# Kernel tuning notes

Measured on AMD Instinct MI355X. Metric: run time of the kernel, lower is better.

The kernel has to match this reference:

```python
import jax, jax.numpy as jnp
import numpy as np

OFF_SLOPE = 0.001

def setup_inputs() -> dict:
    key = jax.random.key(0)
    B, S, I, H = 128, 1024, 128, 256
    ks = jax.random.split(key, 8)
    stdv = 1.0 / np.sqrt(H)
    x = jax.random.normal(ks[0], (B, S, I), dtype=jnp.float32)
    # monotone positive timestamps per sequence
    ts = jnp.sort(jax.random.uniform(ks[1], (B, S), jnp.float32, 0.0, 1000.0), axis=1)
    W = jax.random.uniform(ks[2], (I, 4 * H), jnp.float32, -stdv, stdv)
    U = jax.random.uniform(ks[3], (H, 4 * H), jnp.float32, -stdv, stdv)
    bias = jax.random.uniform(ks[4], (4 * H,), jnp.float32, -stdv, stdv)
    # Periods = exp(2*rand + 1), Shifts ~ U(0,100), On_End = 0.05 (per init_weights)
    Periods = jnp.exp(2.0 * jax.random.uniform(ks[5], (H, 1), jnp.float32) + 1.0)
    Shifts = jax.random.uniform(ks[6], (H, 1), jnp.float32, 0.0, 100.0)
    On_End = jnp.full((H, 1), 0.05, dtype=jnp.float32)
    return {"x": x, "ts": ts, "W": W, "U": U, "bias": bias,
            "Periods": Periods, "Shifts": Shifts, "On_End": On_End}

def reference(x, ts, W, U, bias, Periods, Shifts, On_End):
    B, S, I = x.shape
    H = U.shape[0]
    shift = Shifts.reshape(1, -1)                 # [1,H]
    period = jnp.abs(Periods.reshape(1, -1))      # [1,H]
    on_mid = jnp.abs(On_End.reshape(1, -1)) * 0.5 * period
    on_end = jnp.abs(On_End.reshape(1, -1)) * period

    def step(carry, inp):
        h, c = carry
        x_t, t_t = inp                            # [B,I], [B]
        gates = x_t @ W + h @ U + bias            # [B,4H]
        i_g, f_g, g_g, o_g = jnp.split(gates, 4, axis=-1)
        i_t = jax.nn.sigmoid(i_g)
        f_t = jax.nn.sigmoid(f_g)
        g_t = jnp.tanh(g_g)
        o_t = jax.nn.sigmoid(o_g)
        c_new = f_t * c + i_t * g_t
        h_new = o_t * jnp.tanh(c_new)
        # phased time gate
        in_cycle = jnp.fmod(t_t[:, None] + shift, period)   # [B,H]
        is_up = in_cycle <= on_mid
        is_down = (in_cycle > on_mid) & (in_cycle <= on_end)
        mask = jnp.where(is_up, in_cycle / on_mid,
                         jnp.where(is_down, (on_end - in_cycle) / on_mid,
                                   OFF_SLOPE * (in_cycle / period)))
        c2 = mask * c_new + (1.0 - mask) * c
        h2 = mask * h_new + (1.0 - mask) * h
        return (h2, c2), h2

    h0 = jnp.zeros((B, H), x.dtype)
    c0 = jnp.zeros((B, H), x.dtype)
    (h_T, c_T), hs = jax.lax.scan(
        step, (h0, c0), (jnp.swapaxes(x, 0, 1), jnp.swapaxes(ts, 0, 1)))
    hidden_seq = jnp.swapaxes(hs, 0, 1)           # [B,S,H]
    return hidden_seq, h_T, c_T
```

## Files before the change

kernel.cpp:

```cpp
#include <hip/hip_runtime.h>
#include <cstdint>
#include <cstddef>

#define B_ 128
#define S_ 1024
#define I_ 128
#define H_ 256
#define G4 1024
#define OFF_SLOPE 0.001f

typedef float f32x4 __attribute__((ext_vector_type(4)));
typedef short s16x8 __attribute__((ext_vector_type(8)));

__device__ __forceinline__ unsigned short f2bf_rne(float f) {
    unsigned int u = __builtin_bit_cast(unsigned int, f);
    u += 0x7FFFu + ((u >> 16) & 1u);
    return (unsigned short)(u >> 16);
}
__device__ __forceinline__ float bf2f(unsigned short h) {
    unsigned int u = ((unsigned int)h) << 16;
    return __builtin_bit_cast(float, u);
}
__device__ __forceinline__ float fsigmoid(float x) {
    return 1.0f / (1.0f + __expf(-x));
}
__device__ __forceinline__ float ftanh(float x) {
    return 2.0f / (1.0f + __expf(-2.0f * x)) - 1.0f;
}

template <bool SCANLAYOUT>
__global__ __launch_bounds__(256) void gemm_xw(const float* __restrict__ X,
                                               const float* __restrict__ W,
                                               const float* __restrict__ bias,
                                               float* __restrict__ Gx) {
    __shared__ float A_s[16 * 128];
    const int tid = threadIdx.x;
    const size_t row0 = (size_t)blockIdx.x * 16;

    for (int i = tid; i < 16 * 128; i += 256)
        A_s[i] = X[row0 * I_ + i];
    __syncthreads();

    const float4 bias4 = ((const float4*)bias)[tid];
    float4 acc[16];
#pragma unroll
    for (int r = 0; r < 16; ++r) acc[r] = bias4;

    const float4* W4 = (const float4*)W;
    for (int k = 0; k < I_; ++k) {
        float4 w = W4[k * 256 + tid];
#pragma unroll
        for (int r = 0; r < 16; ++r) {
            float a = A_s[r * 128 + k];
            acc[r].x = fmaf(a, w.x, acc[r].x);
            acc[r].y = fmaf(a, w.y, acc[r].y);
            acc[r].z = fmaf(a, w.z, acc[r].z);
            acc[r].w = fmaf(a, w.w, acc[r].w);
        }
    }
    if (SCANLAYOUT) {
        const int b = (int)(row0 >> 10);
        const int t0 = (int)(row0 & 1023);
        const int g = b >> 4, bb = b & 15;
        const int n0 = 4 * tid;
        const int q = n0 >> 8, u = n0 & 255, cb = u >> 5, j = u & 31;
        const int lc = q * 32 + j;
#pragma unroll
        for (int r = 0; r < 16; ++r) {
            size_t idx = ((((size_t)(g * 8 + cb) * 1024 + (t0 + r)) * 16 + bb) * 128 + lc);
            *(float4*)&Gx[idx] = acc[r];
        }
    } else {
        float4* O4 = (float4*)Gx;
#pragma unroll
        for (int r = 0; r < 16; ++r)
            O4[(row0 + r) * 256 + tid] = acc[r];
    }
}

__global__ __launch_bounds__(256, 1) void plstm_mfma(
    const float* __restrict__ ts, const float* __restrict__ U,
    const float* __restrict__ Periods, const float* __restrict__ Shifts,
    const float* __restrict__ OnEnd, const float* __restrict__ Gx,
    float* __restrict__ out, unsigned long long* __restrict__ hbuf,
    int* __restrict__ ctr) {
    const int blk = blockIdx.x;
    const int g = blk & 7;
    const int cb = blk >> 3;
    const int tid = threadIdx.x;
    const int w = tid >> 6;
    const int l = tid & 63;
    const int lr = l & 15;
    const int lg = l >> 4;

    __shared__ unsigned short h_hi[16 * 264];
    __shared__ unsigned short h_lo[16 * 264];
    __shared__ float gates[4 * 16 * 33];

    s16x8 Uhi[2][8], Ulo[2][8];
#pragma unroll
    for (int tt = 0; tt < 2; ++tt) {
        const int n = w * 256 + cb * 32 + tt * 16 + lr;
#pragma unroll
        for (int kk = 0; kk < 8; ++kk) {
            s16x8 hi8, lo8;
#pragma unroll
            for (int i = 0; i < 8; ++i) {
                int k = kk * 32 + lg * 8 + i;
                float uv = U[(size_t)k * G4 + n];
                unsigned short h = f2bf_rne(uv);
                float r = uv - bf2f(h);
                hi8[i] = (short)h;
                lo8[i] = (short)f2bf_rne(r);
            }
            Uhi[tt][kk] = hi8;
            Ulo[tt][kk] = lo8;
        }
    }

    const int eb = tid >> 4;
    const int ej = 2 * (tid & 15);
    const int u0 = cb * 32 + ej;
    const float per0 = fabsf(Periods[u0]), per1 = fabsf(Periods[u0 + 1]);
    const float sh0 = Shifts[u0], sh1 = Shifts[u0 + 1];
    const float oe0 = fabsf(OnEnd[u0]) * per0, oe1 = fabsf(OnEnd[u0 + 1]) * per1;
    const float om0 = 0.5f * oe0, om1 = 0.5f * oe1;
    const float iom0 = 1.0f / om0, iom1 = 1.0f / om1;
    const float ip0 = 1.0f / per0, ip1 = 1.0f / per1;

    float c0 = 0.f, c1 = 0.f, h0 = 0.f, h1 = 0.f;
    const float* tsrow = ts + (size_t)(g * 16 + eb) * S_;
    const float* gxbase = Gx + (size_t)(g * 8 + cb) * 1024 * 2048 + eb * 128;
    float* outrow = out + (size_t)(g * 16 + eb) * S_ * H_ + u0;

    unsigned long long* const hb0 = hbuf + (size_t)g * 2048;
    unsigned long long* const hb1 = hbuf + (size_t)(8 + g) * 2048;

    for (int i = tid; i < 16 * 264; i += 256) { h_hi[i] = 0; h_lo[i] = 0; }
    __syncthreads();

    const int abase = lr * 264 + lg * 8;
    const int pubidx = eb * 128 + cb * 16 + (tid & 15);
    const int b2 = tid >> 4, seg = tid & 15;
    const int rbase = b2 * 128 + seg * 8;

    float2 cq0 = *(const float2*)&gxbase[0 * 32 + ej];
    float2 cq1 = *(const float2*)&gxbase[1 * 32 + ej];
    float2 cq2 = *(const float2*)&gxbase[2 * 32 + ej];
    float2 cq3 = *(const float2*)&gxbase[3 * 32 + ej];
    float tsc = tsrow[0];

    for (int t = 0; t < S_; ++t) {
        f32x4 a0 = {0.f, 0.f, 0.f, 0.f}, a1 = {0.f, 0.f, 0.f, 0.f};
#pragma unroll
        for (int kk = 0; kk < 8; ++kk) {
            s16x8 ah = *(const s16x8*)&h_hi[abase + kk * 32];
            s16x8 al = *(const s16x8*)&h_lo[abase + kk * 32];
            a0 = __builtin_amdgcn_mfma_f32_16x16x32_bf16(ah, Uhi[0][kk], a0, 0, 0, 0);
            a0 = __builtin_amdgcn_mfma_f32_16x16x32_bf16(ah, Ulo[0][kk], a0, 0, 0, 0);
            a0 = __builtin_amdgcn_mfma_f32_16x16x32_bf16(al, Uhi[0][kk], a0, 0, 0, 0);
            a1 = __builtin_amdgcn_mfma_f32_16x16x32_bf16(ah, Uhi[1][kk], a1, 0, 0, 0);
            a1 = __builtin_amdgcn_mfma_f32_16x16x32_bf16(ah, Ulo[1][kk], a1, 0, 0, 0);
            a1 = __builtin_amdgcn_mfma_f32_16x16x32_bf16(al, Uhi[1][kk], a1, 0, 0, 0);
        }
#pragma unroll
        for (int r = 0; r < 4; ++r) {
            gates[(w * 16 + lg * 4 + r) * 33 + lr] = a0[r];
            gates[(w * 16 + lg * 4 + r) * 33 + 16 + lr] = a1[r];
        }
        __syncthreads();

        float i0 = gates[(0 * 16 + eb) * 33 + ej] + cq0.x;
        float f0 = gates[(1 * 16 + eb) * 33 + ej] + cq1.x;
        float g0 = gates[(2 * 16 + eb) * 33 + ej] + cq2.x;
        float o0 = gates[(3 * 16 + eb) * 33 + ej] + cq3.x;
        float i1 = gates[(0 * 16 + eb) * 33 + ej + 1] + cq0.y;
        float f1 = gates[(1 * 16 + eb) * 33 + ej + 1] + cq1.y;
        float g1 = gates[(2 * 16 + eb) * 33 + ej + 1] + cq2.y;
        float o1 = gates[(3 * 16 + eb) * 33 + ej + 1] + cq3.y;

        float it0 = fsigmoid(i0), ft0 = fsigmoid(f0);
        float gt0 = ftanh(g0), ot0 = fsigmoid(o0);
        float it1 = fsigmoid(i1), ft1 = fsigmoid(f1);
        float gt1 = ftanh(g1), ot1 = fsigmoid(o1);

        float cn0 = fmaf(ft0, c0, it0 * gt0);
        float hn0 = ot0 * ftanh(cn0);
        float cn1 = fmaf(ft1, c1, it1 * gt1);
        float hn1 = ot1 * ftanh(cn1);

        float ic0 = fmodf(tsc + sh0, per0);
        float m0 = (ic0 <= om0) ? ic0 * iom0
                 : (ic0 <= oe0) ? (oe0 - ic0) * iom0
                                : OFF_SLOPE * (ic0 * ip0);
        float ic1 = fmodf(tsc + sh1, per1);
        float m1 = (ic1 <= om1) ? ic1 * iom1
                 : (ic1 <= oe1) ? (oe1 - ic1) * iom1
                                : OFF_SLOPE * (ic1 * ip1);

        c0 = m0 * cn0 + (1.f - m0) * c0;
        c1 = m1 * cn1 + (1.f - m1) * c1;
        h0 = m0 * hn0 + (1.f - m0) * h0;
        h1 = m1 * hn1 + (1.f - m1) * h1;

        *(float2*)&outrow[(size_t)t * H_] = make_float2(h0, h1);

        unsigned int hiw = (unsigned int)f2bf_rne(h0) | ((unsigned int)f2bf_rne(h1) << 16);
        float r0 = h0 - bf2f(f2bf_rne(h0));
        float r1 = h1 - bf2f(f2bf_rne(h1));
        unsigned int low = (unsigned int)f2bf_rne(r0) | ((unsigned int)f2bf_rne(r1) << 16);
        unsigned long long pack = (unsigned long long)hiw |
                                  ((unsigned long long)low << 32);
        unsigned long long* hbp = (t & 1) ? hb1 : hb0;
        __hip_atomic_store(&hbp[pubidx], pack, __ATOMIC_RELAXED,
                           __HIP_MEMORY_SCOPE_AGENT);
        __syncthreads();

        float2 nq0 = cq0, nq1 = cq1, nq2 = cq2, nq3 = cq3;
        float tsn = tsc;
        if (t + 1 < S_) {
            const float* gxn = gxbase + (size_t)(t + 1) * 2048;
            nq0 = *(const float2*)&gxn[0 * 32 + ej];
            nq1 = *(const float2*)&gxn[1 * 32 + ej];
            nq2 = *(const float2*)&gxn[2 * 32 + ej];
            nq3 = *(const float2*)&gxn[3 * 32 + ej];
            tsn = tsrow[t + 1];
        }

        if (tid == 0)
            __hip_atomic_fetch_add(&ctr[t], 1, __ATOMIC_RELAXED,
                                   __HIP_MEMORY_SCOPE_AGENT);
        {
            int guard = 0;
            while (__hip_atomic_load(&ctr[t], __ATOMIC_RELAXED,
                                     __HIP_MEMORY_SCOPE_AGENT) < 8) {
                if (++guard > (1 << 15)) break;
            }
        }
        asm volatile("" ::: "memory");
        __builtin_amdgcn_sched_barrier(0);

        {
            const unsigned long long* src = (t & 1) ? hb1 : hb0;
            unsigned long long v[8];
#pragma unroll
            for (int i = 0; i < 8; ++i)
                v[i] = __hip_atomic_load(&src[rbase + i], __ATOMIC_RELAXED,
                                         __HIP_MEMORY_SCOPE_AGENT);
            uint4 hA, hB, lA, lB;
            hA.x = (unsigned int)v[0]; hA.y = (unsigned int)v[1];
            hA.z = (unsigned int)v[2]; hA.w = (unsigned int)v[3];
            hB.x = (unsigned int)v[4]; hB.y = (unsigned int)v[5];
            hB.z = (unsigned int)v[6]; hB.w = (unsigned int)v[7];
            lA.x = (unsigned int)(v[0] >> 32); lA.y = (unsigned int)(v[1] >> 32);
            lA.z = (unsigned int)(v[2] >> 32); lA.w = (unsigned int)(v[3] >> 32);
            lB.x = (unsigned int)(v[4] >> 32); lB.y = (unsigned int)(v[5] >> 32);
            lB.z = (unsigned int)(v[6] >> 32); lB.w = (unsigned int)(v[7] >> 32);
            const int doff = b2 * 264 + seg * 16;
            *(uint4*)&h_hi[doff] = hA;
            *(uint4*)&h_hi[doff + 8] = hB;
            *(uint4*)&h_lo[doff] = lA;
            *(uint4*)&h_lo[doff + 8] = lB;
        }
        __syncthreads();

        cq0 = nq0; cq1 = nq1; cq2 = nq2; cq3 = nq3; tsc = tsn;
    }

    const size_t fin = (size_t)B_ * S_ * H_;
    *(float2*)&out[fin + (size_t)(g * 16 + eb) * H_ + u0] = make_float2(h0, h1);
    *(float2*)&out[fin + (size_t)B_ * H_ + (size_t)(g * 16 + eb) * H_ + u0] =
        make_float2(c0, c1);
}

template <bool PRE>
__global__ __launch_bounds__(512) void plstm_scan2(
    const float* __restrict__ x, const float* __restrict__ ts,
    const float* __restrict__ W, const float* __restrict__ U,
    const float* __restrict__ bias, const float* __restrict__ Periods,
    const float* __restrict__ Shifts, const float* __restrict__ OnEnd,
    const float* __restrict__ Gx, float* __restrict__ out) {
    const int g = blockIdx.x;
    const int tid = threadIdx.x;
    const int lane = tid & 255;
    const int bb = tid >> 8;
    const int b0 = 2 * g, b1 = 2 * g + 1;
    const int bcur = b0 + bb;

    __shared__ float h_s[2][H_];
    __shared__ float gate_s[2][G4];
    __shared__ float x_s[2][I_];

    const float period = fabsf(Periods[lane]);
    const float shift = Shifts[lane];
    const float oe = fabsf(OnEnd[lane]);
    const float on_mid = oe * 0.5f * period;
    const float on_end = oe * period;
    const float inv_on_mid = 1.0f / on_mid;
    const float inv_period = 1.0f / period;

    ((float*)h_s)[tid] = 0.f;

    float c = 0.f, last_h = 0.f;
    float2 bias2 = make_float2(0.f, 0.f);
    if (!PRE) bias2 = ((const float2*)bias)[tid];

    const float2* W2 = (const float2*)W;
    const float2* U2 = (const float2*)U;
    const float2* Gx2 = (const float2*)Gx;
    const float* tsb = ts + (size_t)bcur * S_;
    const size_t obase = (size_t)bcur * S_ * H_;

    for (int t = 0; t < S_; ++t) {
        if (!PRE) {
            if (tid < 2 * I_)
                x_s[tid >> 7][tid & 127] =
                    x[((size_t)(b0 + (tid >> 7)) * S_ + t) * I_ + (tid & 127)];
        }
        __syncthreads();

        float2 a0, a1;
        if (PRE) {
            a0 = Gx2[((size_t)b0 * S_ + t) * (G4 / 2) + tid];
            a1 = Gx2[((size_t)b1 * S_ + t) * (G4 / 2) + tid];
        } else {
            a0 = bias2; a1 = bias2;
#pragma unroll 8
            for (int k = 0; k < I_; ++k) {
                float2 w = W2[k * (G4 / 2) + tid];
                float x0 = x_s[0][k], x1 = x_s[1][k];
                a0.x = fmaf(x0, w.x, a0.x);
                a0.y = fmaf(x0, w.y, a0.y);
                a1.x = fmaf(x1, w.x, a1.x);
                a1.y = fmaf(x1, w.y, a1.y);
            }
        }
#pragma unroll 8
        for (int k = 0; k < H_; ++k) {
            float2 u = U2[k * (G4 / 2) + tid];
            float hv0 = h_s[0][k], hv1 = h_s[1][k];
            a0.x = fmaf(hv0, u.x, a0.x);
            a0.y = fmaf(hv0, u.y, a0.y);
            a1.x = fmaf(hv1, u.x, a1.x);
            a1.y = fmaf(hv1, u.y, a1.y);
        }
        ((float2*)gate_s[0])[tid] = a0;
        ((float2*)gate_s[1])[tid] = a1;
        __syncthreads();

        {
            float ig = gate_s[bb][lane];
            float fg = gate_s[bb][H_ + lane];
            float gg = gate_s[bb][2 * H_ + lane];
            float og = gate_s[bb][3 * H_ + lane];
            float i_t = 1.f / (1.f + expf(-ig));
            float f_t = 1.f / (1.f + expf(-fg));
            float g_t = tanhf(gg);
            float o_t = 1.f / (1.f + expf(-og));
            float hp = h_s[bb][lane];
            float c_new = fmaf(f_t, c, i_t * g_t);
            float h_new = o_t * tanhf(c_new);

            float tv = tsb[t];
            float in_c = fmodf(tv + shift, period);
            float mask;
            if (in_c <= on_mid) mask = in_c * inv_on_mid;
            else if (in_c <= on_end) mask = (on_end - in_c) * inv_on_mid;
            else mask = OFF_SLOPE * (in_c * inv_period);

            c = mask * c_new + (1.f - mask) * c;
            float h2 = mask * h_new + (1.f - mask) * hp;
            h_s[bb][lane] = h2;
            out[obase + (size_t)t * H_ + lane] = h2;
            last_h = h2;
        }
    }

    out[(size_t)B_ * S_ * H_ + (size_t)bcur * H_ + lane] = last_h;
    out[(size_t)B_ * S_ * H_ + (size_t)B_ * H_ + (size_t)bcur * H_ + lane] = c;
}

extern "C" void kernel_launch(void* const* d_in, const int* in_sizes, int n_in,
                              void* d_out, int out_size, void* d_ws, size_t ws_size,
                              hipStream_t stream) {
    (void)in_sizes; (void)n_in; (void)out_size;
    const float* x = (const float*)d_in[0];
    const float* ts = (const float*)d_in[1];
    const float* W = (const float*)d_in[2];
    const float* U = (const float*)d_in[3];
    const float* bias = (const float*)d_in[4];
    const float* Periods = (const float*)d_in[5];
    const float* Shifts = (const float*)d_in[6];
    const float* OnEnd = (const float*)d_in[7];
    float* out = (float*)d_out;

    const size_t gx_bytes = (size_t)B_ * S_ * G4 * sizeof(float);
    const size_t meta_bytes = 1 << 20;

    if (ws_size >= gx_bytes + meta_bytes) {
        int* ctr = (int*)d_ws;
        unsigned long long* hbuf = (unsigned long long*)((char*)d_ws + 4096);
        float* Gx = (float*)((char*)d_ws + meta_bytes);
        hipMemsetAsync(d_ws, 0, 4096, stream);
        gemm_xw<true><<<(B_ * S_) / 16, 256, 0, stream>>>(x, W, bias, Gx);
        plstm_mfma<<<64, 256, 0, stream>>>(ts, U, Periods, Shifts, OnEnd, Gx,
                                           out, hbuf, ctr);
    } else if (ws_size >= gx_bytes) {
        float* Gx = (float*)d_ws;
        gemm_xw<false><<<(B_ * S_) / 16, 256, 0, stream>>>(x, W, bias, Gx);
        plstm_scan2<true><<<B_ / 2, 512, 0, stream>>>(x, ts, W, U, bias, Periods,
                                                      Shifts, OnEnd, Gx, out);
    } else {
        plstm_scan2<false><<<B_ / 2, 512, 0, stream>>>(x, ts, W, U, bias, Periods,
                                                       Shifts, OnEnd, nullptr, out);
    }
}
```

Measured before the change: 3.811 ms.

## Replace counter barrier with per-element parity flags embedded in published h values

```diff
diff --git a/kernel.cpp b/kernel.cpp
--- a/kernel.cpp
+++ b/kernel.cpp
@@ -82,8 +82,7 @@
     const float* __restrict__ ts, const float* __restrict__ U,
     const float* __restrict__ Periods, const float* __restrict__ Shifts,
     const float* __restrict__ OnEnd, const float* __restrict__ Gx,
-    float* __restrict__ out, unsigned long long* __restrict__ hbuf,
-    int* __restrict__ ctr) {
+    float* __restrict__ out, unsigned long long* __restrict__ hbuf) {
     const int blk = blockIdx.x;
     const int g = blk & 7;
     const int cb = blk >> 3;
@@ -205,16 +204,18 @@
 
         *(float2*)&outrow[(size_t)t * H_] = make_float2(h0, h1);
 
+        const unsigned int want = ((t >> 1) & 1) ? 0x00010001u : 0u;
         unsigned int hiw = (unsigned int)f2bf_rne(h0) | ((unsigned int)f2bf_rne(h1) << 16);
         float r0 = h0 - bf2f(f2bf_rne(h0));
         float r1 = h1 - bf2f(f2bf_rne(h1));
         unsigned int low = (unsigned int)f2bf_rne(r0) | ((unsigned int)f2bf_rne(r1) << 16);
+        low = (low & 0xFFFEFFFEu) | want;
         unsigned long long pack = (unsigned long long)hiw |
                                   ((unsigned long long)low << 32);
-        unsigned long long* hbp = (t & 1) ? hb1 : hb0;
+        unsigned long long* const hbp = (t & 1) ? hb1 : hb0;
         __hip_atomic_store(&hbp[pubidx], pack, __ATOMIC_RELAXED,
                            __HIP_MEMORY_SCOPE_AGENT);
-        __syncthreads();
+        __builtin_amdgcn_sched_barrier(0);
 
         float2 nq0 = cq0, nq1 = cq1, nq2 = cq2, nq3 = cq3;
         float tsn = tsc;
@@ -227,26 +228,24 @@
             tsn = tsrow[t + 1];
         }
 
-        if (tid == 0)
-            __hip_atomic_fetch_add(&ctr[t], 1, __ATOMIC_RELAXED,
-                                   __HIP_MEMORY_SCOPE_AGENT);
-        {
-            int guard = 0;
-            while (__hip_atomic_load(&ctr[t], __ATOMIC_RELAXED,
-                                     __HIP_MEMORY_SCOPE_AGENT) < 8) {
-                if (++guard > (1 << 15)) break;
-            }
-        }
-        asm volatile("" ::: "memory");
-        __builtin_amdgcn_sched_barrier(0);
-
+        unsigned long long v[8];
         {
             const unsigned long long* src = (t & 1) ? hb1 : hb0;
-            unsigned long long v[8];
-#pragma unroll
-            for (int i = 0; i < 8; ++i)
-                v[i] = __hip_atomic_load(&src[rbase + i], __ATOMIC_RELAXED,
-                                         __HIP_MEMORY_SCOPE_AGENT);
+            int guard = 0;
+            bool all;
+            do {
+                all = true;
+#pragma unroll
+                for (int i = 0; i < 8; ++i)
+                    v[i] = __hip_atomic_load(&src[rbase + i], __ATOMIC_RELAXED,
+                                             __HIP_MEMORY_SCOPE_AGENT);
+#pragma unroll
+                for (int i = 0; i < 8; ++i)
+                    all = all && (((unsigned int)(v[i] >> 32) & 0x00010001u) == want);
+            } while (!all && ++guard < (1 << 14));
+        }
+
+        {
             uint4 hA, hB, lA, lB;
             hA.x = (unsigned int)v[0]; hA.y = (unsigned int)v[1];
             hA.z = (unsigned int)v[2]; hA.w = (unsigned int)v[3];
@@ -395,16 +394,16 @@
     float* out = (float*)d_out;
 
     const size_t gx_bytes = (size_t)B_ * S_ * G4 * sizeof(float);
+    const size_t hbuf_bytes = 2 * 8 * 2048 * 8;
     const size_t meta_bytes = 1 << 20;
 
     if (ws_size >= gx_bytes + meta_bytes) {
-        int* ctr = (int*)d_ws;
-        unsigned long long* hbuf = (unsigned long long*)((char*)d_ws + 4096);
+        unsigned long long* hbuf = (unsigned long long*)d_ws;
         float* Gx = (float*)((char*)d_ws + meta_bytes);
-        hipMemsetAsync(d_ws, 0, 4096, stream);
+        hipMemsetAsync(d_ws, 0xFF, hbuf_bytes, stream);
         gemm_xw<true><<<(B_ * S_) / 16, 256, 0, stream>>>(x, W, bias, Gx);
         plstm_mfma<<<64, 256, 0, stream>>>(ts, U, Periods, Shifts, OnEnd, Gx,
-                                           out, hbuf, ctr);
+                                           out, hbuf);
     } else if (ws_size >= gx_bytes) {
         float* Gx = (float*)d_ws;
         gemm_xw<false><<<(B_ * S_) / 16, 256, 0, stream>>>(x, W, bias, Gx);
```

Result: faster. 3.600 ms (-5.5%).
